# Optimization experiments

Measured on AMD Instinct MI355X. Metric: run time of the kernel, lower is better.

## Reference

```python
import jax, jax.numpy as jnp
import numpy as np

B, S, IN_DIM, MEM, LAYERS, HEADS, TOP_K = 64, 256, 512, 256, 3, 8, 200


def setup_inputs() -> dict:
    key = jax.random.key(0)
    ks = jax.random.split(key, 16)
    inputs = jax.random.normal(ks[0], (B, S, IN_DIM), jnp.float32)
    # dependency-style sparse 0/1 adjacency, symmetric with self loops
    a = (jax.random.uniform(ks[1], (B, S, S)) < 0.05).astype(jnp.float32)
    adj = jnp.clip(a + jnp.swapaxes(a, -1, -2) + jnp.eye(S, dtype=jnp.float32), 0.0, 1.0)
    lengths = jnp.maximum(jax.random.randint(ks[2], (B,), 0, S + 1), 32)
    pad = jnp.arange(S)[None, :] >= lengths[:, None]  # [B,S] True at pad positions
    score_mask = pad[:, None, :, None] | pad[:, None, None, :]  # [B,1,S,S]
    d = {"adj": adj, "inputs": inputs, "score_mask": score_mask}

    def lin(k, din, dout):
        k1, k2 = jax.random.split(k)
        s = 1.0 / np.sqrt(din)
        return (jax.random.uniform(k1, (din, dout), jnp.float32, -s, s),
                jax.random.uniform(k2, (dout,), jnp.float32, -s, s))

    ki = 3
    for l in range(LAYERS):
        w, b = lin(ks[ki], IN_DIM + l * MEM, MEM); ki += 1
        d[f"W{l}_w"], d[f"W{l}_b"] = w, b
    for i in range(LAYERS - 1):
        din = IN_DIM + (i + 1) * MEM
        qw, qb = lin(ks[ki], din, din); ki += 1
        kw, kb = lin(ks[ki], din, din); ki += 1
        d[f"attn{i}_qw"], d[f"attn{i}_qb"] = qw, qb
        d[f"attn{i}_kw"], d[f"attn{i}_kb"] = kw, kb
    return d


def _gcn_layer(adj, x, denom, W, b):
    # AxW = W(adj @ x) / denom ; out = relu(AxW) + W(x)   (dropout=identity, eval)
    AxW = ((adj @ x) @ W + b) / denom
    return jax.nn.relu(AxW) + (x @ W + b)


def _mha_adj(x, qw, qb, kw, kb, mask):
    Bn, Sn, D = x.shape
    dk = D // HEADS
    q = (x @ qw + qb).reshape(Bn, Sn, HEADS, dk).transpose(0, 2, 1, 3)
    k = (x @ kw + kb).reshape(Bn, Sn, HEADS, dk).transpose(0, 2, 1, 3)
    scores = jnp.einsum('bhqd,bhkd->bhqk', q, k) / jnp.sqrt(jnp.float32(dk))
    scores = jnp.where(mask, jnp.float32(-1e9), scores)
    keep = (~mask[:, :, :, 0:1]).astype(scores.dtype)  # zero out pad query rows
    return jax.nn.softmax(scores, axis=-1) * keep


def _select(m, top_num):
    # per-batch top-k threshold over flattened [S*S], symmetrize, diag := 1
    Bn, Sn, _ = m.shape
    flat = m.reshape(Bn, -1)
    thr = jax.lax.top_k(flat, top_num)[0][:, -1:]
    sel = (flat >= thr).astype(m.dtype).reshape(Bn, Sn, Sn)
    sel = sel + jnp.swapaxes(sel, -1, -2)
    eye = jnp.eye(Sn, dtype=m.dtype)
    return sel * (1.0 - eye) + eye


def reference(adj, inputs, score_mask, W0_w, W0_b, W1_w, W1_b, W2_w, W2_b,
              attn0_qw, attn0_qb, attn0_kw, attn0_kb,
              attn1_qw, attn1_qb, attn1_kw, attn1_kb):
    Ws = [(W0_w, W0_b), (W1_w, W1_b), (W2_w, W2_b)]
    attns = [(attn0_qw, attn0_qb, attn0_kw, attn0_kb),
             (attn1_qw, attn1_qb, attn1_kw, attn1_kb)]
    denom = adj.sum(2, keepdims=True) + 1.0
    out = _gcn_layer(adj, inputs, denom, *Ws[0])
    x = inputs
    for i in range(1, LAYERS):
        x = jnp.concatenate([x, out], axis=-1)  # growing concatenated features
        a = _mha_adj(x, *attns[i - 1], score_mask)  # [B,H,S,S]
        a = a.sum(axis=1)  # second_layer='sum' branch
        a = _select(a, TOP_K) * a
        denom = a.sum(2, keepdims=True) + 1.0
        out = _gcn_layer(a, x, denom, *Ws[i])
    return out
```

## Files before the change

### kernel.cpp

```cpp
#include <hip/hip_runtime.h>
#include <math.h>


typedef __attribute__((ext_vector_type(8))) short s16x8;
typedef __attribute__((ext_vector_type(4))) short s16x4;
typedef __attribute__((ext_vector_type(4))) float f32x4;

__device__ __forceinline__ short f2bf(float x) {
    unsigned u = __float_as_uint(x);
    u += 0x7FFF + ((u >> 16) & 1);
    return (short)(u >> 16);
}
__device__ __forceinline__ float bf2f(short h) {
    return __uint_as_float(((unsigned)(unsigned short)h) << 16);
}

__device__ __forceinline__ void gl2l(const void* g, void* l) {
    __builtin_amdgcn_global_load_lds(
        (const __attribute__((address_space(1))) unsigned int*)g,
        (__attribute__((address_space(3))) unsigned int*)l, 16, 0, 0);
}

__device__ __forceinline__ float blk_sum(float v, float* sb) {
#pragma unroll
    for (int o = 32; o; o >>= 1) v += __shfl_down(v, o);
    int lane = threadIdx.x & 63, w = threadIdx.x >> 6;
    if (!lane) sb[w] = v;
    __syncthreads();
    float r = sb[0] + sb[1] + sb[2] + sb[3];
    __syncthreads();
    return r;
}

__global__ void init_flags(int* flags) {
    if (threadIdx.x < 3) flags[threadIdx.x] = 0;
}

__global__ void detect_mask(const unsigned int* __restrict__ w, int nwords, int* flags) {
    int stride = gridDim.x * blockDim.x;
    int l_u8 = 0, l_f32 = 0, l_nz = 0;
    for (int i = blockIdx.x * blockDim.x + threadIdx.x; i < nwords; i += stride) {
        unsigned v = w[i];
        if (v) {
            l_nz = 1;
            if (v == 0x3F800000u) l_f32 = 1;
            else if (v > 1u) l_u8 = 1;
        }
    }
    if (__ballot(l_u8) && (threadIdx.x & 63) == 0) atomicOr(&flags[0], 1);
    if (__ballot(l_f32) && (threadIdx.x & 63) == 0) atomicOr(&flags[1], 1);
    if (__ballot(l_nz) && (threadIdx.x & 63) == 0) atomicOr(&flags[2], 1);
}

__global__ void extract_pad(const void* __restrict__ mask, const int* __restrict__ flags,
                            unsigned char* __restrict__ pad) {
    int b = blockIdx.x, i = threadIdx.x;
    int v;
    size_t idx = (size_t)b * 65536 + (size_t)i * 256;
    if (flags[0]) v = ((const unsigned char*)mask)[idx] != 0;
    else if (flags[2]) v = ((const unsigned int*)mask)[idx] != 0;
    else v = 0;
    pad[b * 256 + i] = (unsigned char)v;
}

__global__ void rowsum_plus1(const float* __restrict__ x, float* __restrict__ out) {
    __shared__ float sb[4];
    int row = blockIdx.x;
    float v = x[(size_t)row * 256 + threadIdx.x];
    float r = blk_sum(v, sb);
    if (!threadIdx.x) out[row] = r + 1.f;
}

__global__ void split_mat(const float* __restrict__ src, int ldsrc, int width,
                          short* __restrict__ dh, short* __restrict__ dl, int ldd) {
    int row = blockIdx.x;
    for (int c = threadIdx.x; c < width; c += 256) {
        float v = src[(size_t)row * ldsrc + c];
        short h = f2bf(v);
        dh[(size_t)row * ldd + c] = h;
        dl[(size_t)row * ldd + c] = f2bf(v - bf2f(h));
    }
}

__global__ void transpose_split(const float* __restrict__ in,
                                short* __restrict__ outh, short* __restrict__ outl,
                                int R, int C, int HR, long PSTR, int rowoff, int outld) {
    __shared__ float tile[32][33];
    int c0 = blockIdx.x * 32, r0 = blockIdx.y * 32;
    int tx = threadIdx.x & 31, ty = threadIdx.x >> 5;
    for (int rr = ty; rr < 32; rr += 8)
        tile[rr][tx] = in[(size_t)(r0 + rr) * C + c0 + tx];
    __syncthreads();
    for (int rr = ty; rr < 32; rr += 8) {
        float v = tile[tx][rr];
        int orow = c0 + rr;
        size_t o = (size_t)(orow / HR) * PSTR + (size_t)((orow % HR) + rowoff) * outld + (r0 + tx);
        short h = f2bf(v);
        outh[o] = h;
        outl[o] = f2bf(v - bf2f(h));
    }
}

__global__ void pack_bias2(const float* __restrict__ qb, const float* __restrict__ kb,
                           float* __restrict__ dst, int D) {
    int i = blockIdx.x * 256 + threadIdx.x;
    if (i < D) {
        int p = i / (D / 2), r = i % (D / 2);
        dst[(size_t)p * D + r] = qb[i];
        dst[(size_t)p * D + D / 2 + r] = kb[i];
    }
}

__global__ __launch_bounds__(256) void mgemm(
    const short* __restrict__ Ah, const short* __restrict__ Al,
    const short* __restrict__ Bh, const short* __restrict__ Bl,
    const float* __restrict__ bias,
    float* __restrict__ C, short* __restrict__ Ch, short* __restrict__ Cl,
    short* __restrict__ CTh, short* __restrict__ CTl,
    const float* __restrict__ denom, const unsigned char* __restrict__ padArr,
    int K, int lda, int ldb, int ldc, int coloff, int zdiv,
    long sA1, long sA2, long sB1, long sB2, long sC1, long sC2,
    long sCT, long sD, float alpha, int mode, int skipmode, int swap) {
    int z = blockIdx.z, zq = z / zdiv, zr = z % zdiv;
    int m0, n0;
    if (swap) { m0 = blockIdx.x * 128; n0 = blockIdx.y * 128; }
    else      { m0 = blockIdx.y * 128; n0 = blockIdx.x * 128; }
    if (skipmode == 1 && padArr[m0]) return;
    if (skipmode == 2 && (padArr[zr * 256 + m0] || padArr[zr * 256 + n0])) return;
    const short* Ahb = Ah + (size_t)zq * sA1 + (size_t)zr * sA2;
    const short* Alb = Al + (size_t)zq * sA1 + (size_t)zr * sA2;
    const short* Bhb = Bh + (size_t)zq * sB1 + (size_t)zr * sB2;
    const short* Blb = Bl + (size_t)zq * sB1 + (size_t)zr * sB2;
    size_t offC = (size_t)zq * sC1 + (size_t)zr * sC2;
    __shared__ short lds[16384];
    int t = threadIdx.x;
    int lane = t & 63, w = t >> 6;
    int wm = w >> 1, wn = w & 1;
    f32x4 acc[4][4];
#pragma unroll
    for (int i = 0; i < 4; ++i)
#pragma unroll
        for (int j = 0; j < 4; ++j)
            acc[i][j] = (f32x4){0.f, 0.f, 0.f, 0.f};

    for (int k0 = 0; k0 < K; k0 += 32) {
        __syncthreads();
#pragma unroll
        for (int p = 0; p < 2; ++p) {
            int s = t + p * 256;
            int mi = (s >> 6) * 16 + (s & 15);
            int koff = k0 + ((s >> 4) & 3) * 8;
            size_t oa = (size_t)(m0 + mi) * lda + koff;
            size_t ob = (size_t)(n0 + mi) * ldb + koff;
            gl2l(Ahb + oa, &lds[s * 8]);
            gl2l(Alb + oa, &lds[4096 + s * 8]);
            gl2l(Bhb + ob, &lds[8192 + s * 8]);
            gl2l(Blb + ob, &lds[12288 + s * 8]);
        }
        __syncthreads();
        s16x8 ah[4], al4[4], bh[4], bl4[4];
#pragma unroll
        for (int i = 0; i < 4; ++i) {
            int off = ((wm * 4 + i) * 64 + lane) * 8;
            ah[i] = *(const s16x8*)&lds[off];
            al4[i] = *(const s16x8*)&lds[4096 + off];
        }
#pragma unroll
        for (int j = 0; j < 4; ++j) {
            int off = ((wn * 4 + j) * 64 + lane) * 8;
            bh[j] = *(const s16x8*)&lds[8192 + off];
            bl4[j] = *(const s16x8*)&lds[12288 + off];
        }
#pragma unroll
        for (int i = 0; i < 4; ++i)
#pragma unroll
            for (int j = 0; j < 4; ++j) {
                acc[i][j] = __builtin_amdgcn_mfma_f32_16x16x32_bf16(ah[i], bh[j], acc[i][j], 0, 0, 0);
                acc[i][j] = __builtin_amdgcn_mfma_f32_16x16x32_bf16(ah[i], bl4[j], acc[i][j], 0, 0, 0);
                acc[i][j] = __builtin_amdgcn_mfma_f32_16x16x32_bf16(al4[i], bh[j], acc[i][j], 0, 0, 0);
            }
    }

    int col = lane & 15, quad = lane >> 4;
#pragma unroll
    for (int i = 0; i < 4; ++i)
#pragma unroll
        for (int j = 0; j < 4; ++j) {
            int mg = m0 + wm * 64 + i * 16 + quad * 4;
            int ng = n0 + wn * 64 + j * 16 + col;
            f32x4 v = acc[i][j];
            if (mode == 0) {
                float bz = bias ? bias[ng] : 0.f;
                float o[4];
#pragma unroll
                for (int r = 0; r < 4; ++r) o[r] = v[r] * alpha + bz;
                if (C) {
                    float* Cb = C + offC;
#pragma unroll
                    for (int r = 0; r < 4; ++r)
                        Cb[(size_t)(mg + r) * ldc + coloff + ng] = o[r];
                }
                if (Ch) {
                    short* Chb = Ch + offC;
                    short* Clb = Cl + offC;
#pragma unroll
                    for (int r = 0; r < 4; ++r) {
                        short hh = f2bf(o[r]);
                        Chb[(size_t)(mg + r) * ldc + coloff + ng] = hh;
                        Clb[(size_t)(mg + r) * ldc + coloff + ng] = f2bf(o[r] - bf2f(hh));
                    }
                }
                if (CTh) {
                    size_t cb = (size_t)zr * sCT + (size_t)(mg >> 8) * 65536 + (size_t)ng * 256 + (mg & 255);
                    s16x4 hv, lv;
#pragma unroll
                    for (int r = 0; r < 4; ++r) {
                        short hh = f2bf(o[r]);
                        hv[r] = hh;
                        lv[r] = f2bf(o[r] - bf2f(hh));
                    }
                    *(s16x4*)&CTh[cb] = hv;
                    *(s16x4*)&CTl[cb] = lv;
                }
            } else {
                float bz = bias[ng];
                size_t cb = (size_t)zr * sCT + (size_t)(mg >> 8) * 65536 + (size_t)ng * 256 + (mg & 255);
                s16x4 th = *(const s16x4*)&CTh[cb];
                s16x4 tl = *(const s16x4*)&CTl[cb];
                const float* Db = denom + (size_t)zr * sD;
#pragma unroll
                for (int r = 0; r < 4; ++r) {
                    float sk = bf2f(th[r]) + bf2f(tl[r]);
                    float u = (v[r] + bz) / Db[mg + r];
                    float o = fmaxf(u, 0.f) + sk + bz;
                    if (C) {
                        C[offC + (size_t)(mg + r) * ldc + coloff + ng] = o;
                    } else {
                        short hh = f2bf(o);
                        Ch[offC + (size_t)(mg + r) * ldc + coloff + ng] = hh;
                        Cl[offC + (size_t)(mg + r) * ldc + coloff + ng] = f2bf(o - bf2f(hh));
                    }
                }
            }
        }
}

__global__ __launch_bounds__(256, 2) void qkgemm(
    const short* __restrict__ Ah, const short* __restrict__ Al,
    const short* __restrict__ Bh, const short* __restrict__ Bl,
    const float* __restrict__ bias,
    short* __restrict__ Ch, short* __restrict__ Cl,
    const unsigned char* __restrict__ padArr,
    int K, int lda, int ldb, int ldc) {
    int m0 = blockIdx.x * 128, n0 = blockIdx.y * 256;
    if (padArr[m0]) return;
    __shared__ short lds[16384];
    int t = threadIdx.x;
    int lane = t & 63, w = t >> 6;
    const short* bhp = Bh + (size_t)(n0 + w * 64 + (lane & 15)) * ldb + (lane >> 4) * 8;
    const short* blp = Bl + (size_t)(n0 + w * 64 + (lane & 15)) * ldb + (lane >> 4) * 8;
    f32x4 acc[8][4];
#pragma unroll
    for (int i = 0; i < 8; ++i)
#pragma unroll
        for (int j = 0; j < 4; ++j)
            acc[i][j] = (f32x4){0.f, 0.f, 0.f, 0.f};

    for (int k0 = 0; k0 < K; k0 += 64) {
        __syncthreads();
#pragma unroll
        for (int p = 0; p < 4; ++p) {
            int s = t + p * 256;
            int row = ((s >> 6) & 7) * 16 + (s & 15);
            int koff = k0 + (s >> 9) * 32 + ((s >> 4) & 3) * 8;
            size_t oa = (size_t)(m0 + row) * lda + koff;
            gl2l(Ah + oa, &lds[s * 8]);
            gl2l(Al + oa, &lds[8192 + s * 8]);
        }
        __syncthreads();
#pragma unroll
        for (int kk = 0; kk < 2; ++kk) {
            s16x8 bh[4], bl4[4];
#pragma unroll
            for (int j = 0; j < 4; ++j) {
                size_t ob = (size_t)j * 16 * ldb + (size_t)(k0 + kk * 32);
                bh[j] = *(const s16x8*)(bhp + ob);
                bl4[j] = *(const s16x8*)(blp + ob);
            }
#pragma unroll
            for (int i = 0; i < 8; ++i) {
                int off = ((kk * 8 + i) * 64 + lane) * 8;
                s16x8 ah = *(const s16x8*)&lds[off];
                s16x8 al4 = *(const s16x8*)&lds[8192 + off];
#pragma unroll
                for (int j = 0; j < 4; ++j) {
                    acc[i][j] = __builtin_amdgcn_mfma_f32_16x16x32_bf16(ah, bh[j], acc[i][j], 0, 0, 0);
                    acc[i][j] = __builtin_amdgcn_mfma_f32_16x16x32_bf16(ah, bl4[j], acc[i][j], 0, 0, 0);
                    acc[i][j] = __builtin_amdgcn_mfma_f32_16x16x32_bf16(al4, bh[j], acc[i][j], 0, 0, 0);
                }
            }
        }
    }

    int col = lane & 15, quad = lane >> 4;
#pragma unroll
    for (int i = 0; i < 8; ++i)
#pragma unroll
        for (int j = 0; j < 4; ++j) {
            int mg = m0 + i * 16 + quad * 4;
            int ng = n0 + w * 64 + j * 16 + col;
            float bz = bias[ng];
#pragma unroll
            for (int r = 0; r < 4; ++r) {
                float o = acc[i][j][r] + bz;
                short hh = f2bf(o);
                Ch[(size_t)(mg + r) * ldc + ng] = hh;
                Cl[(size_t)(mg + r) * ldc + ng] = f2bf(o - bf2f(hh));
            }
        }
}

__global__ void softmax_headsum2(const float* __restrict__ scores,
                                 const unsigned char* __restrict__ pad,
                                 float* __restrict__ a, int accum) {
    int row = blockIdx.x * 4 + (threadIdx.x >> 6);
    int lane = threadIdx.x & 63;
    int b = row >> 8;
    float* arow = a + (size_t)row * 256;
    if (pad[row]) {
        if (!accum) ((float4*)arow)[lane] = make_float4(0.f, 0.f, 0.f, 0.f);
        return;
    }
    unsigned pw = *(const unsigned*)(pad + (b << 8) + lane * 4);
    float4 racc;
    if (accum) racc = ((float4*)arow)[lane];
    else racc = make_float4(0.f, 0.f, 0.f, 0.f);
#pragma unroll
    for (int hh = 0; hh < 2; ++hh) {
        float4 s = ((const float4*)(scores + (size_t)hh * 4194304 + (size_t)row * 256))[lane];
        if (pw & 0x000000FFu) s.x = -1e9f;
        if (pw & 0x0000FF00u) s.y = -1e9f;
        if (pw & 0x00FF0000u) s.z = -1e9f;
        if (pw & 0xFF000000u) s.w = -1e9f;
        float m = fmaxf(fmaxf(s.x, s.y), fmaxf(s.z, s.w));
#pragma unroll
        for (int o = 32; o; o >>= 1) m = fmaxf(m, __shfl_xor(m, o));
        float e0 = expf(s.x - m), e1 = expf(s.y - m), e2 = expf(s.z - m), e3 = expf(s.w - m);
        float sum = e0 + e1 + e2 + e3;
#pragma unroll
        for (int o = 32; o; o >>= 1) sum += __shfl_xor(sum, o);
        float inv = 1.f / sum;
        racc.x += e0 * inv; racc.y += e1 * inv; racc.z += e2 * inv; racc.w += e3 * inv;
    }
    ((float4*)arow)[lane] = racc;
}

__global__ void tk_init(unsigned* ghist, unsigned* prefix, int* krem) {
    int i = blockIdx.x * 256 + threadIdx.x;
    ghist[i] = 0;
    if (i < 64) { prefix[i] = 0; krem[i] = 200; }
}

__global__ void tk_hist(const float* __restrict__ a, const unsigned* __restrict__ prefix,
                        unsigned* __restrict__ ghist, int shift) {
    __shared__ unsigned h[256];
    int b = blockIdx.x >> 4, slice = blockIdx.x & 15;
    h[threadIdx.x] = 0;
    __syncthreads();
    unsigned pfx = prefix[b];
    const unsigned* ab = (const unsigned*)(a + (size_t)b * 65536) + slice * 4096;
    for (int i = threadIdx.x; i < 4096; i += 256) {
        unsigned u = ab[i];
        if ((shift == 24) || ((u >> (shift + 8)) == pfx)) atomicAdd(&h[(u >> shift) & 255], 1u);
    }
    __syncthreads();
    if (h[threadIdx.x]) atomicAdd(&ghist[b * 256 + threadIdx.x], h[threadIdx.x]);
}

__global__ void tk_pick(unsigned* __restrict__ ghist, unsigned* __restrict__ prefix,
                        int* __restrict__ krem, float* __restrict__ thr, int last) {
    __shared__ unsigned h[256];
    int b = blockIdx.x;
    h[threadIdx.x] = ghist[b * 256 + threadIdx.x];
    ghist[b * 256 + threadIdx.x] = 0;
    __syncthreads();
    if (!threadIdx.x) {
        int k = krem[b];
        unsigned c = 0;
        int bin = 255;
        for (; bin >= 0; --bin) { c += h[bin]; if ((int)c >= k) break; }
        if (bin < 0) bin = 0;
        krem[b] = k - (int)(c - h[bin]);
        unsigned p = (prefix[b] << 8) | (unsigned)bin;
        prefix[b] = p;
        if (last) thr[b] = __uint_as_float(p);
    }
}

__global__ void select_apply(const float* __restrict__ a, const float* __restrict__ thr,
                             short* __restrict__ a2h, short* __restrict__ a2l,
                             float* __restrict__ denom) {
    __shared__ float sb[4];
    int row = blockIdx.x;
    int b = row >> 8, i = row & 255, j = threadIdx.x;
    const float* ab = a + (size_t)b * 65536;
    float tb = thr[b];
    float v = ab[i * 256 + j];
    float vt = ab[j * 256 + i];
    float sel = (v >= tb ? 1.f : 0.f) + (vt >= tb ? 1.f : 0.f);
    if (i == j) sel = 1.f;
    float av = v * sel;
    short hh = f2bf(av);
    a2h[(size_t)row * 256 + j] = hh;
    a2l[(size_t)row * 256 + j] = f2bf(av - bf2f(hh));
    float r = blk_sum(av, sb);
    if (!j) denom[row] = r + 1.f;
}

extern "C" void kernel_launch(void* const* d_in, const int* in_sizes, int n_in,
                              void* d_out, int out_size, void* d_ws, size_t ws_size,
                              hipStream_t stream) {
    const float* adj = (const float*)d_in[0];
    const float* x0 = (const float*)d_in[1];
    const void* mask = d_in[2];
    const float* Wls[3] = {(const float*)d_in[3], (const float*)d_in[5], (const float*)d_in[7]};
    const float* bls[3] = {(const float*)d_in[4], (const float*)d_in[6], (const float*)d_in[8]};
    const float* qws[2] = {(const float*)d_in[9], (const float*)d_in[13]};
    const float* qbs[2] = {(const float*)d_in[10], (const float*)d_in[14]};
    const float* kws[2] = {(const float*)d_in[11], (const float*)d_in[15]};
    const float* kbs[2] = {(const float*)d_in[12], (const float*)d_in[16]};

    char* base = (char*)d_ws;
    size_t cur = 0;
    auto alloc = [&](size_t bytes) -> void* {
        cur = (cur + 1023) & ~(size_t)1023;
        void* p = base + cur;
        cur += bytes;
        return p;
    };
    const size_t NROW = 16384;
    int* flags = (int*)alloc(12);
    unsigned char* pad = (unsigned char*)alloc(NROW);
    float* denom = (float*)alloc(NROW * 4);
    float* thr = (float*)alloc(256);
    unsigned* prefix = (unsigned*)alloc(256);
    int* krem = (int*)alloc(256);
    unsigned* ghist = (unsigned*)alloc(64 * 256 * 4);
    short* WTh = (short*)alloc((size_t)2304 * 256 * 2);
    short* WTl = (short*)alloc((size_t)2304 * 256 * 2);
    short* qkwPh = (short*)alloc((size_t)2 * 1024 * 1024 * 2);
    short* qkwPl = (short*)alloc((size_t)2 * 1024 * 1024 * 2);
    float* qkb = (float*)alloc((size_t)2 * 1024 * 4);
    short* xh = (short*)alloc(NROW * 1024 * 2);
    short* xl = (short*)alloc(NROW * 1024 * 2);
    char* Sreg = (char*)alloc((size_t)2 * 64 * 65536 * 4);
    float* a = (float*)alloc(NROW * 256 * 4);
    short* a2h = (short*)alloc(NROW * 256 * 2);
    short* a2l = (short*)alloc(NROW * 256 * 2);
    short* QKh = (short*)alloc(NROW * 1024 * 2);
    short* QKl = (short*)alloc(NROW * 1024 * 2);
    if (ws_size < cur) return;

    short* tzTh = (short*)Sreg;
    short* tzTl = (short*)Sreg + (size_t)64 * 65536;
    float* scores = (float*)Sreg;
    short* adjh = QKh;
    short* adjl = QKl;
    const int Ks[3] = {512, 768, 1024};
    const long offW[3] = {0, (long)512 * 256, (long)(512 + 768) * 256};

    init_flags<<<1, 64, 0, stream>>>(flags);
    detect_mask<<<64, 256, 0, stream>>>((const unsigned int*)mask, 1048576, flags);
    extract_pad<<<64, 256, 0, stream>>>(mask, flags, pad);
    rowsum_plus1<<<16384, 256, 0, stream>>>(adj, denom);
    split_mat<<<16384, 256, 0, stream>>>(x0, 512, 512, xh, xl, 1024);
    split_mat<<<16384, 256, 0, stream>>>(adj, 256, 256, adjh, adjl, 256);
    for (int l = 0; l < 3; ++l)
        transpose_split<<<dim3(8, Ks[l] / 32), 256, 0, stream>>>(
            Wls[l], WTh + offW[l], WTl + offW[l], Ks[l], 256, 256, 0, 0, Ks[l]);

    for (int l = 0; l < 3; ++l) {
        int Kl = Ks[l];
        mgemm<<<dim3(128, 2, 1), 256, 0, stream>>>(
            xh, xl, WTh + offW[l], WTl + offW[l], nullptr,
            nullptr, nullptr, nullptr, tzTh, tzTl, nullptr, nullptr,
            Kl, 1024, Kl, 0, 0, 1,
            0, 0, 0, 0, 0, 0, 0, 0, 1.f, 0, 0, 1);
        const short* Aah = (l == 0) ? adjh : a2h;
        const short* Aal = (l == 0) ? adjl : a2l;
        if (l < 2) {
            mgemm<<<dim3(2, 2, 64), 256, 0, stream>>>(
                Aah, Aal, tzTh, tzTl, bls[l],
                nullptr, xh, xl, tzTh, tzTl, denom, nullptr,
                256, 256, 256, 1024, Kl, 64,
                0, 65536, 0, 65536, 0, (long)256 * 1024, 65536, 256, 1.f, 1, 0, 0);
        } else {
            mgemm<<<dim3(2, 2, 64), 256, 0, stream>>>(
                Aah, Aal, tzTh, tzTl, bls[l],
                (float*)d_out, nullptr, nullptr, tzTh, tzTl, denom, nullptr,
                256, 256, 256, 256, 0, 64,
                0, 65536, 0, 65536, 0, 65536, 65536, 256, 1.f, 1, 0, 0);
            break;
        }

        int D = Ks[l + 1], dk = D / 8, HD = D / 2;
        float scale = 1.f / sqrtf((float)dk);
        transpose_split<<<dim3(D / 32, D / 32), 256, 0, stream>>>(
            qws[l], qkwPh, qkwPl, D, D, HD, (long)D * D, 0, D);
        transpose_split<<<dim3(D / 32, D / 32), 256, 0, stream>>>(
            kws[l], qkwPh, qkwPl, D, D, HD, (long)D * D, HD, D);
        pack_bias2<<<4, 256, 0, stream>>>(qbs[l], kbs[l], qkb, D);

        for (int p = 0; p < 2; ++p) {
            qkgemm<<<dim3(128, D / 256), 256, 0, stream>>>(
                xh, xl, qkwPh + (size_t)p * D * D, qkwPl + (size_t)p * D * D,
                qkb + (size_t)p * D, QKh, QKl, pad, D, 1024, D, D);
            for (int hp = 0; hp < 2; ++hp) {
                mgemm<<<dim3(2, 2, 128), 256, 0, stream>>>(
                    QKh + (size_t)(hp * 2) * dk, QKl + (size_t)(hp * 2) * dk,
                    QKh + HD + (size_t)(hp * 2) * dk, QKl + HD + (size_t)(hp * 2) * dk,
                    nullptr, scores, nullptr, nullptr, nullptr, nullptr, nullptr, pad,
                    dk, D, D, 256, 0, 64,
                    dk, (long)256 * D, dk, (long)256 * D, (long)64 * 65536, 65536,
                    0, 0, scale, 0, 2, 0);
                softmax_headsum2<<<4096, 256, 0, stream>>>(scores, pad, a, (p * 2 + hp) ? 1 : 0);
            }
        }
        tk_init<<<64, 256, 0, stream>>>(ghist, prefix, krem);
        for (int pp = 0; pp < 4; ++pp) {
            tk_hist<<<1024, 256, 0, stream>>>(a, prefix, ghist, 24 - 8 * pp);
            tk_pick<<<64, 256, 0, stream>>>(ghist, prefix, krem, thr, pp == 3);
        }
        select_apply<<<16384, 256, 0, stream>>>(a, thr, a2h, a2l, denom);
    }
}
```

Baseline: 1.264 ms.

## Double-buffer A tiles in qkgemm LDS to overlap loads with MFMA

Doubles the qkgemm LDS buffer and prefetches the next K-tile of the A hi/lo operands via global_load_lds while the current tile is consumed by MFMAs, using explicit barriers and vmcnt waits. This hides global-to-LDS latency that the previous single-buffered loop exposed between two syncthreads. LDS use doubles to 64KB per block, which may reduce occupancy below the requested 2 blocks per CU, and the vmcnt(8) count depends on the interleaved B register loads.

```diff
diff --git a/kernel.cpp b/kernel.cpp
--- a/kernel.cpp
+++ b/kernel.cpp
@@ -254,7 +254,7 @@
     int K, int lda, int ldb, int ldc) {
     int m0 = blockIdx.x * 128, n0 = blockIdx.y * 256;
     if (padArr[m0]) return;
-    __shared__ short lds[16384];
+    __shared__ short lds[32768];
     int t = threadIdx.x;
     int lane = t & 63, w = t >> 6;
     const short* bhp = Bh + (size_t)(n0 + w * 64 + (lane & 15)) * ldb + (lane >> 4) * 8;
@@ -266,18 +266,36 @@
         for (int j = 0; j < 4; ++j)
             acc[i][j] = (f32x4){0.f, 0.f, 0.f, 0.f};
 
-    for (int k0 = 0; k0 < K; k0 += 64) {
-        __syncthreads();
-#pragma unroll
-        for (int p = 0; p < 4; ++p) {
-            int s = t + p * 256;
-            int row = ((s >> 6) & 7) * 16 + (s & 15);
-            int koff = k0 + (s >> 9) * 32 + ((s >> 4) & 3) * 8;
-            size_t oa = (size_t)(m0 + row) * lda + koff;
-            gl2l(Ah + oa, &lds[s * 8]);
-            gl2l(Al + oa, &lds[8192 + s * 8]);
-        }
-        __syncthreads();
+#define QK_STAGE(bi, kbase)                                         \
+    do {                                                            \
+        int base_ = (bi) << 14;                                     \
+        _Pragma("unroll")                                           \
+        for (int p = 0; p < 4; ++p) {                               \
+            int s = t + p * 256;                                    \
+            int row = ((s >> 6) & 7) * 16 + (s & 15);               \
+            int koff = (kbase) + (s >> 9) * 32 + ((s >> 4) & 3) * 8;\
+            size_t oa = (size_t)(m0 + row) * lda + koff;            \
+            gl2l(Ah + oa, &lds[base_ + s * 8]);                     \
+            gl2l(Al + oa, &lds[base_ + 8192 + s * 8]);              \
+        }                                                           \
+    } while (0)
+
+    int nt = K >> 6;
+    QK_STAGE(0, 0);
+    for (int tt = 0; tt < nt; ++tt) {
+        asm volatile("" ::: "memory");
+        __builtin_amdgcn_s_barrier();
+        asm volatile("" ::: "memory");
+        if (tt + 1 < nt) {
+            QK_STAGE((tt + 1) & 1, (tt + 1) * 64);
+            asm volatile("s_waitcnt vmcnt(8)" ::: "memory");
+        } else {
+            asm volatile("s_waitcnt vmcnt(0)" ::: "memory");
+        }
+        __builtin_amdgcn_s_barrier();
+        asm volatile("" ::: "memory");
+        int base = (tt & 1) << 14;
+        int k0 = tt * 64;
 #pragma unroll
         for (int kk = 0; kk < 2; ++kk) {
             s16x8 bh[4], bl4[4];
@@ -289,7 +307,7 @@
             }
 #pragma unroll
             for (int i = 0; i < 8; ++i) {
-                int off = ((kk * 8 + i) * 64 + lane) * 8;
+                int off = base + ((kk * 8 + i) * 64 + lane) * 8;
                 s16x8 ah = *(const s16x8*)&lds[off];
                 s16x8 al4 = *(const s16x8*)&lds[8192 + off];
 #pragma unroll
@@ -301,6 +319,7 @@
             }
         }
     }
+#undef QK_STAGE
 
     int col = lane & 15, quad = lane >> 4;
 #pragma unroll
```

Result: slower. 1.316 ms (+4.1%).
